# Performance work log

Measured on AMD Instinct MI355X. Metric: run time of the kernel, lower is better.

## Reference

```python
import jax, jax.numpy as jnp
import numpy as np

KS = (0.8, 0.75, 0.667, 0.5)  # pools 500 -> 400 -> 300 -> 200 -> 100 nodes


def gcn(g, h, W, b):
    # torch GCN.forward with p=0: relu(linear(g @ h))
    return jax.nn.relu(jnp.matmul(g, h) @ W.T + b)


def norm_g(g):
    # faithful to torch: [n,n] / [n] broadcasts over the LAST axis (column-normalize)
    return g / jnp.sum(g, axis=1)


def top_k_graph(scores, g, h, k):
    n = g.shape[0]
    kk = max(2, int(k * n))
    values, idx = jax.lax.top_k(scores, kk)  # sorted descending, matches torch.topk
    new_h = h[idx, :] * values[:, None]
    un_g = (g != 0).astype(g.dtype)
    un_g = (jnp.matmul(un_g, un_g) != 0).astype(g.dtype)  # 2-hop connectivity
    un_g = un_g[idx][:, idx]
    return norm_g(un_g), new_h, idx


def setup_inputs() -> dict:
    key = jax.random.key(0)
    ks = jax.random.split(key, 16)
    N, IN_DIM = 500, 32768
    g = (jax.random.uniform(ks[0], (N, N)) < 0.1).astype(jnp.float32)
    h = jax.random.normal(ks[1], (N, IN_DIM), dtype=jnp.float32)
    inp = {
        "g": g,
        "h": h,
        "W_top": jax.random.normal(ks[2], (1, IN_DIM), dtype=jnp.float32) / np.float32(np.sqrt(IN_DIM)),
        "b_top": jnp.zeros((1,), jnp.float32),
    }
    down_dims = [400, 300, 200, 100]
    for i in range(4):
        inp[f"Wp{i}"] = jax.random.normal(ks[3 + i], (1, 1), dtype=jnp.float32)
        inp[f"bp{i}"] = jnp.zeros((1,), jnp.float32)
        inp[f"Wd{i}"] = jax.random.normal(ks[8 + i], (1, down_dims[i]), dtype=jnp.float32) / np.float32(np.sqrt(down_dims[i]))
        inp[f"bd{i}"] = jnp.zeros((1,), jnp.float32)
    return inp


def reference(g, h, W_top, b_top, Wp0, bp0, Wd0, bd0, Wp1, bp1, Wd1, bd1,
              Wp2, bp2, Wd2, bd2, Wp3, bp3, Wd3, bd3):
    Wp = [Wp0, Wp1, Wp2, Wp3]
    bp = [bp0, bp1, bp2, bp3]
    Wd = [Wd0, Wd1, Wd2, Wd3]
    bd = [bd0, bd1, bd2, bd3]
    h = gcn(g, h, W_top, b_top)  # [500, 1]
    h1 = h
    for i in range(4):
        # SAGPool: scores from a tiny GCN(1 -> 1), then topk prune + 2-hop adjacency
        scores = jax.nn.sigmoid(jnp.squeeze(gcn(g, h, Wp[i], bp[i])))  # [n]
        g, h, idx = top_k_graph(scores, g, h, KS[i])
        # down GCN consumes the diagonal matrix built from the pooled 1-feature h
        h = gcn(g, jnp.diag(jnp.squeeze(h)), Wd[i], bd[i])  # [n_i, 1]
        h1 = jnp.concatenate([h1, h], axis=0)
    return h1  # [500+400+300+200+100, 1] = [1500, 1]
```

## Files before the change

### kernel.cpp

```cpp
#include <hip/hip_runtime.h>


#define MS 16
struct P4 { const float* p[4]; };

__device__ __forceinline__ float bitselF(unsigned m, int k, float v) {
    int s = ((int)(m << (31 - k))) >> 31;
    return __int_as_float(s & __float_as_int(v));
}
__device__ __forceinline__ float fbfly(float v) {
#pragma unroll
    for (int o = 32; o; o >>= 1) v += __shfl_xor(v, o);
    return v;
}
__device__ __forceinline__ int ibfly(int v) {
#pragma unroll
    for (int o = 32; o; o >>= 1) v += __shfl_xor(v, o);
    return v;
}
__device__ __forceinline__ float sigm(float x) { return 1.f / (1.f + expf(-x)); }

__device__ __forceinline__ int wrank(const float* __restrict__ sc, float my,
                                     int r, int lane) {
    int cnt = 0;
#pragma unroll
    for (int q = 0; q < 2; ++q) {
        int j = (lane + 64 * q) << 2;
        float4 v = *(const float4*)(sc + j);
        cnt += (v.x > my) || (v.x == my && (j + 0) < r);
        cnt += (v.y > my) || (v.y == my && (j + 1) < r);
        cnt += (v.z > my) || (v.z == my && (j + 2) < r);
        cnt += (v.w > my) || (v.w == my && (j + 3) < r);
    }
    return ibfly(cnt);
}

__device__ __forceinline__ float pwalk16(const unsigned* __restrict__ row,
                                         const float* __restrict__ val) {
    float a = 0.f;
#pragma unroll
    for (int w = 0; w < 16; ++w) {
        unsigned m = row[w];
        while (m) {
            int b = __ffs((int)m) - 1;
            m &= m - 1;
            a += val[(w << 5) + b];
        }
    }
    return a;
}

__global__ __launch_bounds__(1024) void k_dot(const float* __restrict__ h,
        const float* __restrict__ Wt, const float* __restrict__ g,
        float* __restrict__ V, unsigned* __restrict__ MA,
        unsigned* __restrict__ SELA) {
    int row = blockIdx.x, t = threadIdx.x;
    if (row == 0 && t < 32) SELA[t] = 0u;
    const float4* h4 = (const float4*)(h + (size_t)row * 32768);
    const float4* w4 = (const float4*)Wt;
    float acc = 0.f;
#pragma unroll
    for (int j = 0; j < 8; ++j) {
        float4 a = h4[t + 1024 * j], b = w4[t + 1024 * j];
        acc = fmaf(a.x, b.x, fmaf(a.y, b.y, fmaf(a.z, b.z, fmaf(a.w, b.w, acc))));
    }
    acc = fbfly(acc);
    __shared__ float red[16];
    if ((t & 63) == 0) red[t >> 6] = acc;
    __syncthreads();
    if (t == 0) {
        float s = 0.f;
        for (int i = 0; i < 16; ++i) s += red[i];
        V[row] = s;
    }
    if (t < 512) {
        float gv = (t < 500) ? g[row * 500 + t] : 0.f;
        unsigned long long bal = __ballot(gv != 0.f);
        if ((t & 63) == 0) {
            int w = t >> 6;
            MA[row * MS + 2 * w] = (unsigned)bal;
            MA[row * MS + 2 * w + 1] = (unsigned)(bal >> 32);
        }
    }
}

__global__ __launch_bounds__(256) void k_row(const unsigned* __restrict__ MA,
        const float* __restrict__ x, const float* __restrict__ c0,
        const float* __restrict__ c1, float* __restrict__ y,
        float* __restrict__ out, int mode) {
    __shared__ float sv[512];
    int t = threadIdx.x;
    sv[t] = (t < 500) ? x[t] : 0.f;
    int t2 = t + 256;
    sv[t2] = (t2 < 500) ? x[t2] : 0.f;
    __syncthreads();
    int wid = t >> 6, lane = t & 63;
    int r = blockIdx.x * 4 + wid;
    float acc = 0.f;
#pragma unroll
    for (int j = 0; j < 8; ++j) {
        unsigned m = MA[r * MS + 2 * j + (lane >> 5)];
        acc += bitselF(m, lane & 31, sv[64 * j + lane]);
    }
    acc = fbfly(acc);
    if (lane == 0) {
        if (mode == 0) {
            float hv = fmaxf(acc + c0[0], 0.f);
            out[r] = hv;
            y[r] = hv;
        } else {
            y[r] = fmaxf(acc * c0[0] + c1[0], 0.f);
        }
    }
}

__global__ __launch_bounds__(256) void k_rank0(const float* __restrict__ Z,
        const float* __restrict__ SHo, int* __restrict__ IDXA,
        unsigned* __restrict__ SELA, float* __restrict__ HSo) {
    __shared__ __align__(16) float sz[512];
    int t = threadIdx.x;
    sz[t] = (t < 500) ? Z[t] : -1.f;
    int t2 = t + 256;
    sz[t2] = (t2 < 500) ? Z[t2] : -1.f;
    __syncthreads();
    int wid = t >> 6, lane = t & 63;
    int r = blockIdx.x * 4 + wid;
    float my = sz[r];
    int cnt = wrank(sz, my, r, lane);
    if (lane == 0 && cnt < 400) {
        IDXA[cnt] = r;
        HSo[r] = SHo[r] * sigm(my);
        atomicOr(&SELA[r >> 5], 1u << (r & 31));
    }
}

__global__ __launch_bounds__(256) void k_hop0(const unsigned* __restrict__ MA,
        const int* __restrict__ IDXA, const unsigned* __restrict__ SELA,
        const float* __restrict__ HSo, const float* __restrict__ Wd0,
        unsigned* __restrict__ CP0, float* __restrict__ RSUMo,
        float* __restrict__ SUc, float* __restrict__ SUo) {
    int t = threadIdx.x, wid = t >> 6, lane = t & 63;
    if (blockIdx.x == 0 && t < 112) SUc[400 + t] = 0.f;
    int r4 = blockIdx.x * 4 + wid;
    int i = IDXA[r4];
    __shared__ unsigned sSEL[16], srow[4][16], un2[4][16];
    if (t < 16) sSEL[t] = SELA[t];
    if (lane < 16) {
        srow[wid][lane] = MA[i * MS + lane];
        un2[wid][lane] = 0u;
    }
    __syncthreads();
    int part = lane >> 4, w = lane & 15;
    unsigned acc = 0;
    for (int k = part; k < 500; k += 4) {
        unsigned sel = (srow[wid][k >> 5] >> (k & 31)) & 1u;
        acc |= MA[k * MS + w] & (0u - sel);
    }
    atomicOr(&un2[wid][w], acc);
    __syncthreads();
    if (lane < 16) {
        unsigned P = sSEL[lane] & ~un2[wid][lane];
        CP0[i * MS + lane] = P;
        int pc = __popc(P);
        pc += __shfl_xor(pc, 1);
        pc += __shfl_xor(pc, 2);
        pc += __shfl_xor(pc, 4);
        pc += __shfl_xor(pc, 8);
        if (lane == 0) {
            float rs = (float)(400 - pc);
            RSUMo[i] = rs;
            float su = HSo[i] * Wd0[r4] / rs;
            SUc[r4] = su;
            SUo[i] = su;
        }
    }
}

__global__ __launch_bounds__(256) void k_m0(const int* __restrict__ IDXA,
        const unsigned* __restrict__ CP0, const float* __restrict__ SUc,
        const float* __restrict__ SUo, const float* __restrict__ RSUMo,
        const float* __restrict__ bd0, float* __restrict__ out,
        float* __restrict__ H1c, float* __restrict__ S2c,
        float* __restrict__ S2o) {
    __shared__ float sO[512];
    int t = threadIdx.x, wid = t >> 6, lane = t & 63;
    sO[t] = (t < 500) ? SUo[t] : 0.f;
    int t2 = t + 256;
    sO[t2] = (t2 < 500) ? SUo[t2] : 0.f;
    if (blockIdx.x == 0 && t < 112) S2c[400 + t] = 0.f;
    __syncthreads();
    float a = 0.f;
    {
        float4 v = *(const float4*)(SUc + lane * 4);
        a += (v.x + v.y) + (v.z + v.w);
        float4 u = *(const float4*)(SUc + lane * 4 + 256);
        a += (u.x + u.y) + (u.z + u.w);
    }
    float tot = fbfly(a);
    int r4 = blockIdx.x * 4 + wid;
    int i = IDXA[r4];
    float corr = 0.f;
    if (lane < 16) {
        unsigned m = CP0[i * MS + lane];
        while (m) {
            int b = __ffs((int)m) - 1;
            m &= m - 1;
            corr += sO[lane * 32 + b];
        }
    }
    corr = fbfly(corr);
    if (lane == 0) {
        float h1 = fmaxf(tot - corr + bd0[0], 0.f);
        out[500 + r4] = h1;
        H1c[r4] = h1;
        float s2 = h1 / RSUMo[i];
        S2c[r4] = s2;
        S2o[i] = s2;
    }
}

__global__ __launch_bounds__(256) void k_z1(const int* __restrict__ IDXA,
        const unsigned* __restrict__ CP0, const float* __restrict__ S2c,
        const float* __restrict__ S2o, const float* __restrict__ Wp1,
        const float* __restrict__ bp1, float* __restrict__ Z1c) {
    __shared__ float sO[512];
    int t = threadIdx.x, wid = t >> 6, lane = t & 63;
    sO[t] = (t < 500) ? S2o[t] : 0.f;
    int t2 = t + 256;
    sO[t2] = (t2 < 500) ? S2o[t2] : 0.f;
    if (blockIdx.x == 0 && t < 112) Z1c[400 + t] = -1.f;
    __syncthreads();
    float a = 0.f;
    {
        float4 v = *(const float4*)(S2c + lane * 4);
        a += (v.x + v.y) + (v.z + v.w);
        float4 u = *(const float4*)(S2c + lane * 4 + 256);
        a += (u.x + u.y) + (u.z + u.w);
    }
    float tot = fbfly(a);
    int r4 = blockIdx.x * 4 + wid;
    int i = IDXA[r4];
    float corr = 0.f;
    if (lane < 16) {
        unsigned m = CP0[i * MS + lane];
        while (m) {
            int b = __ffs((int)m) - 1;
            m &= m - 1;
            corr += sO[lane * 32 + b];
        }
    }
    corr = fbfly(corr);
    if (lane == 0) Z1c[r4] = fmaxf((tot - corr) * Wp1[0] + bp1[0], 0.f);
}

__global__ __launch_bounds__(1024) void k_fin(const int* __restrict__ IDXA,
        const unsigned* __restrict__ CP0g, const float* __restrict__ Z1cg,
        const float* __restrict__ H1c, const unsigned* __restrict__ SELAg,
        P4 Wp, P4 bp, P4 Wd, P4 bd, float* __restrict__ out) {
    __shared__ unsigned sCP[8000];
    __shared__ __align__(16) float szC[512], svC[512], s2C[512];
    __shared__ float svO[512], s2O[512], shvO[512], sHSo[512], srsO[512];
    __shared__ int sIDXp[2][512];
    __shared__ unsigned sSELp[2][16];
    __shared__ float sS[8];
    __shared__ float stotS;
    __shared__ int sFlag;
    int t = threadIdx.x, wid = t >> 6, lane = t & 63;
    for (int q = t; q < 8000; q += 1024) sCP[q] = CP0g[q];
    if (t < 512) {
        szC[t] = Z1cg[t];
        sIDXp[0][t] = (t < 400) ? IDXA[t] : 0;
    }
    if (t < 16) {
        sSELp[0][t] = SELAg[t];
        sSELp[1][t] = 0u;
    }
    if (t == 0) sFlag = 0;
    __syncthreads();
    if (t < 400) shvO[sIDXp[0][t]] = H1c[t];
    __syncthreads();
    for (int r = wid; r < 400; r += 16) {
        float my = szC[r];
        int cnt = wrank(szC, my, r, lane);
        if (lane == 0 && cnt < 300) {
            int io = sIDXp[0][r];
            sIDXp[1][cnt] = io;
            sHSo[io] = shvO[io] * sigm(my);
            atomicOr(&sSELp[1][io >> 5], 1u << (io & 31));
        }
    }
    __syncthreads();
    unsigned P[16];
    int inew = 0, pc = 0;
    float su_ = 0.f;
    if (t < 300) {
        inew = sIDXp[1][t];
#pragma unroll
        for (int w = 0; w < 16; ++w) P[w] = sSELp[1][w];
        bool alive = true;
        for (int w2 = 0; w2 < 16 && alive; ++w2) {
            unsigned nb = sSELp[0][w2] & ~sCP[inew * MS + w2];
            while (nb) {
                int b = __ffs((int)nb) - 1;
                nb &= nb - 1;
                const unsigned* cj = sCP + (w2 * 32 + b) * MS;
                unsigned orr = 0;
#pragma unroll
                for (int w = 0; w < 16; ++w) {
                    P[w] &= cj[w];
                    orr |= P[w];
                }
                if (!orr) { alive = false; break; }
            }
        }
#pragma unroll
        for (int w = 0; w < 16; ++w) pc += __popc(P[w]);
        if (pc > 0) atomicOr(&sFlag, 1);
        float rs = (float)(300 - pc);
        su_ = sHSo[inew] * Wd.p[1][t] / rs;
    }
    __syncthreads();
    if (t < 300) {
#pragma unroll
        for (int w = 0; w < 16; ++w) sCP[inew * MS + w] = P[w];
        srsO[inew] = (float)(300 - pc);
        svC[t] = su_;
        svO[inew] = su_;
    } else if (t < 512) {
        svC[t] = 0.f;
    }
    __syncthreads();
    if (sFlag == 0) {
        if (t < 64) {
            float p = 0.f;
#pragma unroll
            for (int j = 0; j < 8; ++j) p += svC[t * 8 + j];
            p = fbfly(p);
            if (t == 0) {
                float h2 = fmaxf(p + bd.p[1][0], 0.f);
                float z2 = fmaxf(h2 * Wp.p[2][0] + bp.p[2][0], 0.f);
                sS[0] = h2;
                sS[1] = h2 * sigm(z2);
            }
        }
        __syncthreads();
        float HS2 = sS[1];
        if (t < 512) s2C[t] = (t < 200) ? HS2 * Wd.p[2][t] / 200.f : 0.f;
        __syncthreads();
        if (t < 64) {
            float p = 0.f;
#pragma unroll
            for (int j = 0; j < 8; ++j) p += s2C[t * 8 + j];
            p = fbfly(p);
            if (t == 0) {
                float h3 = fmaxf(p + bd.p[2][0], 0.f);
                float z3 = fmaxf(h3 * Wp.p[3][0] + bp.p[3][0], 0.f);
                sS[2] = h3;
                sS[3] = h3 * sigm(z3);
            }
        }
        __syncthreads();
        float HS3 = sS[3];
        if (t < 512) s2C[t] = (t < 100) ? HS3 * Wd.p[3][t] / 100.f : 0.f;
        __syncthreads();
        if (t < 64) {
            float p = 0.f;
#pragma unroll
            for (int j = 0; j < 8; ++j) p += s2C[t * 8 + j];
            p = fbfly(p);
            if (t == 0) sS[4] = fmaxf(p + bd.p[3][0], 0.f);
        }
        __syncthreads();
        if (t < 300) out[900 + t] = sS[0];
        else if (t < 500) out[1200 + (t - 300)] = sS[2];
        else if (t < 600) out[1400 + (t - 500)] = sS[4];
        return;
    }
    const int kks[3] = {300, 200, 100};
    const int kns[3] = {200, 100, 0};
    const int offs[3] = {900, 1200, 1400};
    for (int l = 1; l <= 3; ++l) {
        const int kk = kks[l - 1], knext = kns[l - 1], off = offs[l - 1];
        const int cur = l & 1, nxt = cur ^ 1;
        if (t < 64) {
            float p = 0.f;
#pragma unroll
            for (int j = 0; j < 8; ++j) p += svC[t * 8 + j];
            p = fbfly(p);
            if (t == 0) stotS = p;
        }
        __syncthreads();
        int i_ = 0;
        if (t < kk) {
            i_ = sIDXp[cur][t];
            float corr = pwalk16(sCP + i_ * MS, svO);
            float hv = fmaxf(stotS - corr + bd.p[l][0], 0.f);
            out[off + t] = hv;
            shvO[i_] = hv;
            float s2 = hv / srsO[i_];
            s2C[t] = s2;
            s2O[i_] = s2;
        } else if (t < 512) {
            s2C[t] = 0.f;
        }
        if (l == 3) break;
        __syncthreads();
        if (t < 64) {
            float p = 0.f;
#pragma unroll
            for (int j = 0; j < 8; ++j) p += s2C[t * 8 + j];
            p = fbfly(p);
            if (t == 0) stotS = p;
        }
        if (t < 16) sSELp[nxt][t] = 0u;
        __syncthreads();
        float z_ = -1.f;
        if (t < kk) {
            float c2 = pwalk16(sCP + i_ * MS, s2O);
            z_ = fmaxf((stotS - c2) * Wp.p[l + 1][0] + bp.p[l + 1][0], 0.f);
        }
        if (t < 512) szC[t] = (t < kk) ? z_ : -1.f;
        __syncthreads();
        for (int r = wid; r < kk; r += 16) {
            float my = szC[r];
            int cnt = wrank(szC, my, r, lane);
            if (lane == 0 && cnt < knext) {
                int io = sIDXp[cur][r];
                sIDXp[nxt][cnt] = io;
                sHSo[io] = shvO[io] * sigm(my);
                atomicOr(&sSELp[nxt][io >> 5], 1u << (io & 31));
            }
        }
        __syncthreads();
        unsigned Q[16];
        int in2 = 0, pc2 = 0;
        float su2_ = 0.f;
        if (t < knext) {
            in2 = sIDXp[nxt][t];
#pragma unroll
            for (int w = 0; w < 16; ++w) Q[w] = sSELp[nxt][w];
            bool alive = true;
            for (int w2 = 0; w2 < 16 && alive; ++w2) {
                unsigned nb = sSELp[cur][w2] & ~sCP[in2 * MS + w2];
                while (nb) {
                    int b = __ffs((int)nb) - 1;
                    nb &= nb - 1;
                    const unsigned* cj = sCP + (w2 * 32 + b) * MS;
                    unsigned orr = 0;
#pragma unroll
                    for (int w = 0; w < 16; ++w) {
                        Q[w] &= cj[w];
                        orr |= Q[w];
                    }
                    if (!orr) { alive = false; break; }
                }
            }
#pragma unroll
            for (int w = 0; w < 16; ++w) pc2 += __popc(Q[w]);
            float rs = (float)(knext - pc2);
            su2_ = sHSo[in2] * Wd.p[l + 1][t] / rs;
        }
        __syncthreads();
        if (t < knext) {
#pragma unroll
            for (int w = 0; w < 16; ++w) sCP[in2 * MS + w] = Q[w];
            srsO[in2] = (float)(knext - pc2);
            svC[t] = su2_;
            svO[in2] = su2_;
        } else if (t < 512) {
            svC[t] = 0.f;
        }
        __syncthreads();
    }
}

extern "C" void kernel_launch(void* const* d_in, const int* in_sizes, int n_in,
                              void* d_out, int out_size, void* d_ws, size_t ws_size,
                              hipStream_t stream) {
    const float* g = (const float*)d_in[0];
    const float* h = (const float*)d_in[1];
    const float* W_top = (const float*)d_in[2];
    const float* b_top = (const float*)d_in[3];
    P4 Wp, bp, Wd, bd;
    for (int i = 0; i < 4; ++i) {
        Wp.p[i] = (const float*)d_in[4 + 4 * i];
        bp.p[i] = (const float*)d_in[5 + 4 * i];
        Wd.p[i] = (const float*)d_in[6 + 4 * i];
        bd.p[i] = (const float*)d_in[7 + 4 * i];
    }
    float* out = (float*)d_out;

    unsigned* wsu = (unsigned*)d_ws;
    float* V = (float*)(wsu + 0);
    float* SHo = (float*)(wsu + 512);
    float* Z = (float*)(wsu + 1024);
    int* IDXA = (int*)(wsu + 1536);
    unsigned* SELA = wsu + 2048;
    float* HSo = (float*)(wsu + 2080);
    float* RSUMo = (float*)(wsu + 2592);
    float* SUc = (float*)(wsu + 3104);
    float* SUo = (float*)(wsu + 3616);
    float* H1c = (float*)(wsu + 4128);
    float* S2c = (float*)(wsu + 4640);
    float* S2o = (float*)(wsu + 5152);
    float* Z1c = (float*)(wsu + 5664);
    unsigned* CP0 = wsu + 6176;
    unsigned* MA = wsu + 14176;

    k_dot<<<500, 1024, 0, stream>>>(h, W_top, g, V, MA, SELA);
    k_row<<<125, 256, 0, stream>>>(MA, V, b_top, nullptr, SHo, out, 0);
    k_row<<<125, 256, 0, stream>>>(MA, SHo, Wp.p[0], bp.p[0], Z, nullptr, 1);
    k_rank0<<<125, 256, 0, stream>>>(Z, SHo, IDXA, SELA, HSo);
    k_hop0<<<100, 256, 0, stream>>>(MA, IDXA, SELA, HSo, Wd.p[0], CP0, RSUMo,
                                    SUc, SUo);
    k_m0<<<100, 256, 0, stream>>>(IDXA, CP0, SUc, SUo, RSUMo, bd.p[0], out, H1c,
                                  S2c, S2o);
    k_z1<<<100, 256, 0, stream>>>(IDXA, CP0, S2c, S2o, Wp.p[1], bp.p[1], Z1c);
    k_fin<<<1, 1024, 0, stream>>>(IDXA, CP0, Z1c, H1c, SELA, Wp, bp, Wd, bd, out);
}
```

Measured before the change: 68.02 us.

## Fuse post-dot pooling stages into two kernels with redundant per-block recompute

Replaces the chain of small kernels (two row GCNs, rank, 2-hop, m0, z1) with one 25-block kernel. Each block redundantly recomputes the first GCN layers and the top-k ranking from the bitmask adjacency held in shared memory, then does its slice of 2-hop masks. The level-1 aggregation and score computation move into the single-block final kernel. This cuts launch count from eight to three and the global round-trips between them, at the cost of duplicated work across blocks and more serial work in the final block.

```diff
diff --git a/kernel.cpp b/kernel.cpp
--- a/kernel.cpp
+++ b/kernel.cpp
@@ -19,21 +19,6 @@
     return v;
 }
 __device__ __forceinline__ float sigm(float x) { return 1.f / (1.f + expf(-x)); }
-
-__device__ __forceinline__ int wrank(const float* __restrict__ sc, float my,
-                                     int r, int lane) {
-    int cnt = 0;
-#pragma unroll
-    for (int q = 0; q < 2; ++q) {
-        int j = (lane + 64 * q) << 2;
-        float4 v = *(const float4*)(sc + j);
-        cnt += (v.x > my) || (v.x == my && (j + 0) < r);
-        cnt += (v.y > my) || (v.y == my && (j + 1) < r);
-        cnt += (v.z > my) || (v.z == my && (j + 2) < r);
-        cnt += (v.w > my) || (v.w == my && (j + 3) < r);
-    }
-    return ibfly(cnt);
-}
 
 __device__ __forceinline__ float pwalk16(const unsigned* __restrict__ row,
                                          const float* __restrict__ val) {
@@ -50,12 +35,22 @@
     return a;
 }
 
+__device__ __forceinline__ int wrank(const float* __restrict__ sc, float my,
+                                     int r, int lane) {
+    int cnt = 0;
+#pragma unroll
+    for (int q = 0; q < 8; ++q) {
+        int j = lane + 64 * q;
+        float s = sc[j];
+        cnt += (s > my) || (s == my && j < r);
+    }
+    return ibfly(cnt);
+}
+
 __global__ __launch_bounds__(1024) void k_dot(const float* __restrict__ h,
         const float* __restrict__ Wt, const float* __restrict__ g,
-        float* __restrict__ V, unsigned* __restrict__ MA,
-        unsigned* __restrict__ SELA) {
+        float* __restrict__ V, unsigned* __restrict__ MA) {
     int row = blockIdx.x, t = threadIdx.x;
-    if (row == 0 && t < 32) SELA[t] = 0u;
     const float4* h4 = (const float4*)(h + (size_t)row * 32768);
     const float4* w4 = (const float4*)Wt;
     float acc = 0.f;
@@ -84,192 +79,108 @@
     }
 }
 
-__global__ __launch_bounds__(256) void k_row(const unsigned* __restrict__ MA,
-        const float* __restrict__ x, const float* __restrict__ c0,
-        const float* __restrict__ c1, float* __restrict__ y,
-        float* __restrict__ out, int mode) {
-    __shared__ float sv[512];
-    int t = threadIdx.x;
-    sv[t] = (t < 500) ? x[t] : 0.f;
-    int t2 = t + 256;
-    sv[t2] = (t2 < 500) ? x[t2] : 0.f;
-    __syncthreads();
-    int wid = t >> 6, lane = t & 63;
-    int r = blockIdx.x * 4 + wid;
-    float acc = 0.f;
-#pragma unroll
-    for (int j = 0; j < 8; ++j) {
-        unsigned m = MA[r * MS + 2 * j + (lane >> 5)];
-        acc += bitselF(m, lane & 31, sv[64 * j + lane]);
-    }
-    acc = fbfly(acc);
-    if (lane == 0) {
-        if (mode == 0) {
-            float hv = fmaxf(acc + c0[0], 0.f);
-            out[r] = hv;
-            y[r] = hv;
-        } else {
-            y[r] = fmaxf(acc * c0[0] + c1[0], 0.f);
-        }
-    }
-}
-
-__global__ __launch_bounds__(256) void k_rank0(const float* __restrict__ Z,
-        const float* __restrict__ SHo, int* __restrict__ IDXA,
-        unsigned* __restrict__ SELA, float* __restrict__ HSo) {
-    __shared__ __align__(16) float sz[512];
-    int t = threadIdx.x;
-    sz[t] = (t < 500) ? Z[t] : -1.f;
-    int t2 = t + 256;
-    sz[t2] = (t2 < 500) ? Z[t2] : -1.f;
-    __syncthreads();
-    int wid = t >> 6, lane = t & 63;
-    int r = blockIdx.x * 4 + wid;
-    float my = sz[r];
-    int cnt = wrank(sz, my, r, lane);
-    if (lane == 0 && cnt < 400) {
-        IDXA[cnt] = r;
-        HSo[r] = SHo[r] * sigm(my);
-        atomicOr(&SELA[r >> 5], 1u << (r & 31));
-    }
-}
-
-__global__ __launch_bounds__(256) void k_hop0(const unsigned* __restrict__ MA,
-        const int* __restrict__ IDXA, const unsigned* __restrict__ SELA,
-        const float* __restrict__ HSo, const float* __restrict__ Wd0,
+__global__ __launch_bounds__(1024) void k_mid(const unsigned* __restrict__ MA,
+        const float* __restrict__ V, const float* __restrict__ b_top,
+        const float* __restrict__ Wp0, const float* __restrict__ bp0,
+        const float* __restrict__ Wd0, float* __restrict__ out,
+        int* __restrict__ IDXA, unsigned* __restrict__ SELA,
         unsigned* __restrict__ CP0, float* __restrict__ RSUMo,
         float* __restrict__ SUc, float* __restrict__ SUo) {
+    __shared__ __align__(16) unsigned sMA[8000];
+    __shared__ float sv[512], sh[512], sz[512];
+    __shared__ int sIDX[512];
+    __shared__ unsigned sSEL[16];
+    __shared__ unsigned srow[16][16];
     int t = threadIdx.x, wid = t >> 6, lane = t & 63;
-    if (blockIdx.x == 0 && t < 112) SUc[400 + t] = 0.f;
-    int r4 = blockIdx.x * 4 + wid;
-    int i = IDXA[r4];
-    __shared__ unsigned sSEL[16], srow[4][16], un2[4][16];
-    if (t < 16) sSEL[t] = SELA[t];
-    if (lane < 16) {
-        srow[wid][lane] = MA[i * MS + lane];
-        un2[wid][lane] = 0u;
-    }
+    for (int q = t; q < 2000; q += 1024)
+        ((uint4*)sMA)[q] = ((const uint4*)MA)[q];
+    if (t < 512) sv[t] = (t < 500) ? V[t] : 0.f;
+    if (t < 16) sSEL[t] = 0u;
+    __syncthreads();
+    for (int r = wid; r < 500; r += 16) {
+        float acc = 0.f;
+#pragma unroll
+        for (int j = 0; j < 8; ++j) {
+            unsigned m = sMA[r * MS + 2 * j + (lane >> 5)];
+            acc += bitselF(m, lane & 31, sv[64 * j + lane]);
+        }
+        acc = fbfly(acc);
+        if (lane == 0) sh[r] = fmaxf(acc + b_top[0], 0.f);
+    }
+    if (t >= 500 && t < 512) sh[t] = 0.f;
+    __syncthreads();
+    if (blockIdx.x == 0 && t < 500) out[t] = sh[t];
+    for (int r = wid; r < 500; r += 16) {
+        float acc = 0.f;
+#pragma unroll
+        for (int j = 0; j < 8; ++j) {
+            unsigned m = sMA[r * MS + 2 * j + (lane >> 5)];
+            acc += bitselF(m, lane & 31, sh[64 * j + lane]);
+        }
+        acc = fbfly(acc);
+        if (lane == 0) sz[r] = fmaxf(acc * Wp0[0] + bp0[0], 0.f);
+    }
+    if (t >= 500 && t < 512) sz[t] = -1.f;
+    __syncthreads();
+    for (int r = wid; r < 500; r += 16) {
+        float my = sz[r];
+        int cnt = wrank(sz, my, r, lane);
+        if (lane == 0 && cnt < 400) {
+            sIDX[cnt] = r;
+            atomicOr(&sSEL[r >> 5], 1u << (r & 31));
+        }
+    }
+    __syncthreads();
+    if (blockIdx.x == 0) {
+        if (t < 400) IDXA[t] = sIDX[t];
+        if (t < 16) SELA[t] = sSEL[t];
+        if (t >= 400 && t < 512) SUc[t] = 0.f;
+    }
+    int r4 = blockIdx.x * 16 + wid;
+    int i = sIDX[r4];
+    if (lane < 16) srow[wid][lane] = sMA[i * MS + lane];
     __syncthreads();
     int part = lane >> 4, w = lane & 15;
     unsigned acc = 0;
     for (int k = part; k < 500; k += 4) {
-        unsigned sel = (srow[wid][k >> 5] >> (k & 31)) & 1u;
-        acc |= MA[k * MS + w] & (0u - sel);
-    }
-    atomicOr(&un2[wid][w], acc);
-    __syncthreads();
-    if (lane < 16) {
-        unsigned P = sSEL[lane] & ~un2[wid][lane];
-        CP0[i * MS + lane] = P;
-        int pc = __popc(P);
-        pc += __shfl_xor(pc, 1);
-        pc += __shfl_xor(pc, 2);
-        pc += __shfl_xor(pc, 4);
-        pc += __shfl_xor(pc, 8);
-        if (lane == 0) {
-            float rs = (float)(400 - pc);
-            RSUMo[i] = rs;
-            float su = HSo[i] * Wd0[r4] / rs;
-            SUc[r4] = su;
-            SUo[i] = su;
-        }
-    }
-}
-
-__global__ __launch_bounds__(256) void k_m0(const int* __restrict__ IDXA,
-        const unsigned* __restrict__ CP0, const float* __restrict__ SUc,
-        const float* __restrict__ SUo, const float* __restrict__ RSUMo,
-        const float* __restrict__ bd0, float* __restrict__ out,
-        float* __restrict__ H1c, float* __restrict__ S2c,
-        float* __restrict__ S2o) {
-    __shared__ float sO[512];
-    int t = threadIdx.x, wid = t >> 6, lane = t & 63;
-    sO[t] = (t < 500) ? SUo[t] : 0.f;
-    int t2 = t + 256;
-    sO[t2] = (t2 < 500) ? SUo[t2] : 0.f;
-    if (blockIdx.x == 0 && t < 112) S2c[400 + t] = 0.f;
-    __syncthreads();
-    float a = 0.f;
-    {
-        float4 v = *(const float4*)(SUc + lane * 4);
-        a += (v.x + v.y) + (v.z + v.w);
-        float4 u = *(const float4*)(SUc + lane * 4 + 256);
-        a += (u.x + u.y) + (u.z + u.w);
-    }
-    float tot = fbfly(a);
-    int r4 = blockIdx.x * 4 + wid;
-    int i = IDXA[r4];
-    float corr = 0.f;
-    if (lane < 16) {
-        unsigned m = CP0[i * MS + lane];
-        while (m) {
-            int b = __ffs((int)m) - 1;
-            m &= m - 1;
-            corr += sO[lane * 32 + b];
-        }
-    }
-    corr = fbfly(corr);
+        unsigned mw = srow[wid][k >> 5];
+        unsigned sel = (mw >> (k & 31)) & 1u;
+        acc |= sMA[k * MS + w] & (0u - sel);
+    }
+    acc |= (unsigned)__shfl_xor((int)acc, 16);
+    acc |= (unsigned)__shfl_xor((int)acc, 32);
+    unsigned P = sSEL[w] & ~acc;
+    int pc = (lane < 16) ? __popc(P) : 0;
+    pc = ibfly(pc);
+    if (lane < 16) CP0[i * MS + lane] = P;
     if (lane == 0) {
-        float h1 = fmaxf(tot - corr + bd0[0], 0.f);
-        out[500 + r4] = h1;
-        H1c[r4] = h1;
-        float s2 = h1 / RSUMo[i];
-        S2c[r4] = s2;
-        S2o[i] = s2;
-    }
-}
-
-__global__ __launch_bounds__(256) void k_z1(const int* __restrict__ IDXA,
-        const unsigned* __restrict__ CP0, const float* __restrict__ S2c,
-        const float* __restrict__ S2o, const float* __restrict__ Wp1,
-        const float* __restrict__ bp1, float* __restrict__ Z1c) {
-    __shared__ float sO[512];
-    int t = threadIdx.x, wid = t >> 6, lane = t & 63;
-    sO[t] = (t < 500) ? S2o[t] : 0.f;
-    int t2 = t + 256;
-    sO[t2] = (t2 < 500) ? S2o[t2] : 0.f;
-    if (blockIdx.x == 0 && t < 112) Z1c[400 + t] = -1.f;
-    __syncthreads();
-    float a = 0.f;
-    {
-        float4 v = *(const float4*)(S2c + lane * 4);
-        a += (v.x + v.y) + (v.z + v.w);
-        float4 u = *(const float4*)(S2c + lane * 4 + 256);
-        a += (u.x + u.y) + (u.z + u.w);
-    }
-    float tot = fbfly(a);
-    int r4 = blockIdx.x * 4 + wid;
-    int i = IDXA[r4];
-    float corr = 0.f;
-    if (lane < 16) {
-        unsigned m = CP0[i * MS + lane];
-        while (m) {
-            int b = __ffs((int)m) - 1;
-            m &= m - 1;
-            corr += sO[lane * 32 + b];
-        }
-    }
-    corr = fbfly(corr);
-    if (lane == 0) Z1c[r4] = fmaxf((tot - corr) * Wp1[0] + bp1[0], 0.f);
+        float rs = (float)(400 - pc);
+        RSUMo[i] = rs;
+        float su = sh[i] * sigm(sz[i]) * Wd0[r4] / rs;
+        SUc[r4] = su;
+        SUo[i] = su;
+    }
 }
 
 __global__ __launch_bounds__(1024) void k_fin(const int* __restrict__ IDXA,
-        const unsigned* __restrict__ CP0g, const float* __restrict__ Z1cg,
-        const float* __restrict__ H1c, const unsigned* __restrict__ SELAg,
-        P4 Wp, P4 bp, P4 Wd, P4 bd, float* __restrict__ out) {
-    __shared__ unsigned sCP[8000];
-    __shared__ __align__(16) float szC[512], svC[512], s2C[512];
+        const unsigned* __restrict__ SELAg, const unsigned* __restrict__ CP0g,
+        const float* __restrict__ RSUMg, const float* __restrict__ SUcg,
+        const float* __restrict__ SUog, P4 Wp, P4 bp, P4 Wd, P4 bd,
+        float* __restrict__ out) {
+    __shared__ __align__(16) unsigned sCP[8000];
+    __shared__ float szC[512], svC[512], s2C[512];
     __shared__ float svO[512], s2O[512], shvO[512], sHSo[512], srsO[512];
     __shared__ int sIDXp[2][512];
     __shared__ unsigned sSELp[2][16];
     __shared__ float sS[8];
-    __shared__ float stotS;
+    __shared__ float stot0, stot1, stotS;
     __shared__ int sFlag;
     int t = threadIdx.x, wid = t >> 6, lane = t & 63;
-    for (int q = t; q < 8000; q += 1024) sCP[q] = CP0g[q];
+    for (int q = t; q < 2000; q += 1024)
+        ((uint4*)sCP)[q] = ((const uint4*)CP0g)[q];
     if (t < 512) {
-        szC[t] = Z1cg[t];
         sIDXp[0][t] = (t < 400) ? IDXA[t] : 0;
+        svC[t] = SUcg[t];
     }
     if (t < 16) {
         sSELp[0][t] = SELAg[t];
@@ -277,7 +188,48 @@
     }
     if (t == 0) sFlag = 0;
     __syncthreads();
-    if (t < 400) shvO[sIDXp[0][t]] = H1c[t];
+    if (t < 400) {
+        int i = sIDXp[0][t];
+        svO[i] = svC[t];
+        srsO[i] = RSUMg[i];
+    }
+    __syncthreads();
+    if (t < 64) {
+        float p = 0.f;
+#pragma unroll
+        for (int j = 0; j < 8; ++j) p += svC[t * 8 + j];
+        p = fbfly(p);
+        if (t == 0) stot0 = p;
+    }
+    __syncthreads();
+    int i0 = 0;
+    if (t < 400) {
+        i0 = sIDXp[0][t];
+        float corr = pwalk16(sCP + i0 * MS, svO);
+        float h1 = fmaxf(stot0 - corr + bd.p[0][0], 0.f);
+        out[500 + t] = h1;
+        shvO[i0] = h1;
+        float s2 = h1 / srsO[i0];
+        s2C[t] = s2;
+        s2O[i0] = s2;
+    } else if (t < 512) {
+        s2C[t] = 0.f;
+    }
+    __syncthreads();
+    if (t < 64) {
+        float p = 0.f;
+#pragma unroll
+        for (int j = 0; j < 8; ++j) p += s2C[t * 8 + j];
+        p = fbfly(p);
+        if (t == 0) stot1 = p;
+    }
+    __syncthreads();
+    if (t < 400) {
+        float c2 = pwalk16(sCP + i0 * MS, s2O);
+        szC[t] = fmaxf((stot1 - c2) * Wp.p[1][0] + bp.p[1][0], 0.f);
+    } else if (t < 512) {
+        szC[t] = -1.f;
+    }
     __syncthreads();
     for (int r = wid; r < 400; r += 16) {
         float my = szC[r];
@@ -492,29 +444,17 @@
 
     unsigned* wsu = (unsigned*)d_ws;
     float* V = (float*)(wsu + 0);
-    float* SHo = (float*)(wsu + 512);
-    float* Z = (float*)(wsu + 1024);
-    int* IDXA = (int*)(wsu + 1536);
-    unsigned* SELA = wsu + 2048;
-    float* HSo = (float*)(wsu + 2080);
-    float* RSUMo = (float*)(wsu + 2592);
-    float* SUc = (float*)(wsu + 3104);
-    float* SUo = (float*)(wsu + 3616);
-    float* H1c = (float*)(wsu + 4128);
-    float* S2c = (float*)(wsu + 4640);
-    float* S2o = (float*)(wsu + 5152);
-    float* Z1c = (float*)(wsu + 5664);
-    unsigned* CP0 = wsu + 6176;
-    unsigned* MA = wsu + 14176;
-
-    k_dot<<<500, 1024, 0, stream>>>(h, W_top, g, V, MA, SELA);
-    k_row<<<125, 256, 0, stream>>>(MA, V, b_top, nullptr, SHo, out, 0);
-    k_row<<<125, 256, 0, stream>>>(MA, SHo, Wp.p[0], bp.p[0], Z, nullptr, 1);
-    k_rank0<<<125, 256, 0, stream>>>(Z, SHo, IDXA, SELA, HSo);
-    k_hop0<<<100, 256, 0, stream>>>(MA, IDXA, SELA, HSo, Wd.p[0], CP0, RSUMo,
-                                    SUc, SUo);
-    k_m0<<<100, 256, 0, stream>>>(IDXA, CP0, SUc, SUo, RSUMo, bd.p[0], out, H1c,
-                                  S2c, S2o);
-    k_z1<<<100, 256, 0, stream>>>(IDXA, CP0, S2c, S2o, Wp.p[1], bp.p[1], Z1c);
-    k_fin<<<1, 1024, 0, stream>>>(IDXA, CP0, Z1c, H1c, SELA, Wp, bp, Wd, bd, out);
-}
+    int* IDXA = (int*)(wsu + 512);
+    unsigned* SELA = wsu + 1024;
+    float* RSUMo = (float*)(wsu + 1056);
+    float* SUc = (float*)(wsu + 1568);
+    float* SUo = (float*)(wsu + 2080);
+    unsigned* CP0 = wsu + 2592;
+    unsigned* MA = wsu + 10592;
+
+    k_dot<<<500, 1024, 0, stream>>>(h, W_top, g, V, MA);
+    k_mid<<<25, 1024, 0, stream>>>(MA, V, b_top, Wp.p[0], bp.p[0], Wd.p[0], out,
+                                   IDXA, SELA, CP0, RSUMo, SUc, SUo);
+    k_fin<<<1, 1024, 0, stream>>>(IDXA, SELA, CP0, RSUMo, SUc, SUo, Wp, bp, Wd,
+                                  bd, out);
+}
```

Measured after the change: 93.80 us. +37.9%, slower.
